# Kernel tuning notes

Measured on AMD Instinct MI355X. Metric: run time of the kernel, lower is better.

The kernel has to match this reference:

```python
import jax, jax.numpy as jnp
import numpy as np

B, S, D = 2, 2048, 2048
H = 16
HD = D // H  # 128
THETA = 10000.0


def setup_inputs() -> dict:
    key = jax.random.key(0)
    ks = jax.random.split(key, 5)
    return {
        "hidden_states": jax.random.normal(ks[0], (B, S, D), dtype=jnp.float32),
        "Wq": jax.random.normal(ks[1], (D, D), dtype=jnp.float32) * 0.02,
        "Wk": jax.random.normal(ks[2], (D, D), dtype=jnp.float32) * 0.02,
        "Wv": jax.random.normal(ks[3], (D, D), dtype=jnp.float32) * 0.02,
        "Wo": jax.random.normal(ks[4], (D, D), dtype=jnp.float32) * 0.02,
    }


def _rotate_half(x):
    x1, x2 = x[..., : HD // 2], x[..., HD // 2:]
    return jnp.concatenate([-x2, x1], axis=-1)


def _rope_cos_sin(seq_len, dtype):
    # freqs = 1/theta^(2i/d), i in [0, d/2)
    inv_freq = 1.0 / (THETA ** (jnp.arange(0, HD, 2, dtype=jnp.float32) / HD))
    ang = jnp.arange(seq_len, dtype=jnp.float32)[:, None] * inv_freq[None, :]  # [S, HD/2]
    cos = jnp.cos(ang).astype(dtype)
    sin = jnp.sin(ang).astype(dtype)
    # torch code does cos.repeat(1,1,1,2): tile halves -> [S, HD]
    cos2 = jnp.concatenate([cos, cos], axis=-1)[None, None]  # [1,1,S,HD]
    sin2 = jnp.concatenate([sin, sin], axis=-1)[None, None]
    return cos2, sin2


def reference(hidden_states, Wq, Wk, Wv, Wo):
    b, s, d = hidden_states.shape
    scale = 1.0 / np.sqrt(HD)
    # torch Linear: y = x @ W.T
    def proj(W):
        y = jnp.einsum("bsd,ed->bse", hidden_states, W)
        return y.reshape(b, s, H, HD).transpose(0, 2, 1, 3)  # [b,h,s,hd]
    q, k, v = proj(Wq), proj(Wk), proj(Wv)

    cos, sin = _rope_cos_sin(s, q.dtype)
    q = q * cos + _rotate_half(q) * sin
    k = k * cos + _rotate_half(k) * sin

    scores = jnp.einsum("bhqd,bhkd->bhqk", q, k) * scale
    # causal mask: -inf strictly above diagonal (kv_len == seq_len here)
    causal = jnp.triu(jnp.full((s, s), -jnp.inf, dtype=scores.dtype), k=1)
    scores = scores + causal[None, None]

    attn = jax.nn.softmax(scores.astype(jnp.float32), axis=-1).astype(q.dtype)
    ctx = jnp.einsum("bhqk,bhkd->bhqd", attn, v)
    ctx = ctx.transpose(0, 2, 1, 3).reshape(b, s, d)
    return jnp.einsum("bsd,ed->bse", ctx, Wo)
```

## Files before the change

### kernel.cpp

```cpp
#include <hip/hip_runtime.h>

typedef unsigned short ushort_t;
typedef __bf16 bf16x8 __attribute__((ext_vector_type(8)));
typedef float f32x4 __attribute__((ext_vector_type(4)));

#define S_LEN 2048
#define DMODEL 2048
#define NH 16
#define HDIM 128
#define BATCH 2
#define M_ROWS (BATCH * S_LEN)

__device__ __forceinline__ ushort_t f2bf(float f) {
    union { float f; unsigned u; } v; v.f = f;
    unsigned r = (v.u + 0x7fffu + ((v.u >> 16) & 1u)) >> 16;
    return (ushort_t)r;
}
__device__ __forceinline__ float bf2f(ushort_t u) {
    union { unsigned u; float f; } v; v.u = ((unsigned)u) << 16;
    return v.f;
}

__device__ __forceinline__ void async16(const void* g, void* l) {
    __builtin_amdgcn_global_load_lds(
        (const __attribute__((address_space(1))) void*)g,
        (__attribute__((address_space(3))) void*)l, 16, 0, 0);
}

__global__ void cvt_bf16(const float* __restrict__ in, ushort_t* __restrict__ out, int n4) {
    int i = blockIdx.x * blockDim.x + threadIdx.x;
    if (i >= n4) return;
    float4 f = ((const float4*)in)[i];
    ushort4 u;
    u.x = f2bf(f.x); u.y = f2bf(f.y); u.z = f2bf(f.z); u.w = f2bf(f.w);
    ((ushort4*)out)[i] = u;
}

__global__ void cvt4_bf16(const float* __restrict__ w0, const float* __restrict__ w1,
                          const float* __restrict__ w2, const float* __restrict__ w3,
                          ushort_t* __restrict__ out, int n4) {
    int i = blockIdx.x * blockDim.x + threadIdx.x;
    if (i >= n4) return;
    int which = blockIdx.y;
    const float* src = which == 0 ? w0 : which == 1 ? w1 : which == 2 ? w2 : w3;
    float4 f = ((const float4*)src)[i];
    ushort4 u;
    u.x = f2bf(f.x); u.y = f2bf(f.y); u.z = f2bf(f.z); u.w = f2bf(f.w);
    ((ushort4*)(out + (size_t)which * DMODEL * DMODEL))[i] = u;
}

__global__ void rope_tables(float* __restrict__ cosT, float* __restrict__ sinT) {
    int i = blockIdx.x * blockDim.x + threadIdx.x;
    int s = i >> 6, f = i & 63;
    float inv = powf(10000.0f, -(float)(2 * f) / 128.0f);
    float ang = (float)s * inv;
    cosT[i] = cosf(ang);
    sinT[i] = sinf(ang);
}

__global__ void rope_inplace(ushort_t* __restrict__ Q, ushort_t* __restrict__ K,
                             const float* __restrict__ cosT, const float* __restrict__ sinT) {
    long i = (long)blockIdx.x * blockDim.x + threadIdx.x;
    int f = (int)(i & 63);
    long t = i >> 6;
    int s = (int)(t & (S_LEN - 1));
    int bh = (int)(t >> 11);
    long base = ((long)bh * S_LEN + s) * HDIM;
    float c = cosT[s * 64 + f], sn = sinT[s * 64 + f];
    float a0 = bf2f(Q[base + f]), a1 = bf2f(Q[base + 64 + f]);
    Q[base + f]      = f2bf(a0 * c - a1 * sn);
    Q[base + 64 + f] = f2bf(a1 * c + a0 * sn);
    float b0 = bf2f(K[base + f]), b1 = bf2f(K[base + 64 + f]);
    K[base + f]      = f2bf(b0 * c - b1 * sn);
    K[base + 64 + f] = f2bf(b1 * c + b0 * sn);
}

__global__ __launch_bounds__(512) void gemm_qkv(
    const ushort_t* __restrict__ A, const ushort_t* __restrict__ Bm,
    ushort_t* __restrict__ Cq, ushort_t* __restrict__ Ck, ushort_t* __restrict__ Cv,
    int K) {
    __shared__ __align__(16) ushort_t As[2][256 * 64];
    __shared__ __align__(16) ushort_t Bs[2][192 * 64];
    const int tid = threadIdx.x;
    const int lane = tid & 63;
    const int w = tid >> 6;
    const int wm = w >> 2, wn = w & 3;
    const int fr = lane & 15, g = lane >> 4;
    const int xcd = blockIdx.x & 7;
    const int local = blockIdx.x >> 3;
    const int brow = (local >> 2) * 256;
    const int bcol = (xcd * 4 + (local & 3)) * 192;

    const ushort_t* aSrc[4];
    const ushort_t* bSrc[3];
    int aDst[4], bDst[3];
#pragma unroll
    for (int q = 0; q < 4; q++) {
        int d = (q * 512 + tid) * 16;
        int row = d >> 7;
        int s = d ^ ((row & 7) << 4);
        aSrc[q] = A + (long)(brow + row) * K + ((s & 127) >> 1);
        aDst[q] = (q * 512 + tid) * 8;
    }
#pragma unroll
    for (int q = 0; q < 3; q++) {
        int d = (q * 512 + tid) * 16;
        int row = d >> 7;
        int s = d ^ ((row & 7) << 4);
        bSrc[q] = Bm + (long)(bcol + row) * K + ((s & 127) >> 1);
        bDst[q] = (q * 512 + tid) * 8;
    }

    f32x4 acc[8][3];
#pragma unroll
    for (int m = 0; m < 8; m++)
#pragma unroll
        for (int n = 0; n < 3; n++) acc[m][n] = (f32x4){0.f, 0.f, 0.f, 0.f};

    auto stageEarly = [&](int buf, int k0) {
        async16(aSrc[0] + k0, &As[buf][aDst[0]]);
        async16(aSrc[2] + k0, &As[buf][aDst[2]]);
#pragma unroll
        for (int q = 0; q < 3; q++) async16(bSrc[q] + k0, &Bs[buf][bDst[q]]);
    };
    auto stageLate = [&](int buf, int k0) {
        async16(aSrc[1] + k0, &As[buf][aDst[1]]);
        async16(aSrc[3] + k0, &As[buf][aDst[3]]);
    };
    auto rdA = [&](int buf, int m, int ks) -> bf16x8 {
        int row = wm * 128 + m * 16 + fr;
        int cb = (ks * 64 + g * 16) ^ ((row & 7) << 4);
        return *(const bf16x8*)((const char*)&As[buf][0] + row * 128 + cb);
    };
    auto rdB = [&](int buf, int n, int ks) -> bf16x8 {
        int row = wn * 48 + n * 16 + fr;
        int cb = (ks * 64 + g * 16) ^ ((row & 7) << 4);
        return *(const bf16x8*)((const char*)&Bs[buf][0] + row * 128 + cb);
    };

    const int NT = K / 64;
    stageEarly(0, 0);  stageLate(0, 0);
    stageEarly(1, 64); stageLate(1, 64);

    for (int kt = 0; kt < NT; ++kt) {
        const int cur = kt & 1;
        if (kt + 1 < NT) asm volatile("s_waitcnt vmcnt(7)" ::: "memory");
        else             asm volatile("s_waitcnt vmcnt(0)" ::: "memory");
        __builtin_amdgcn_sched_barrier(0);
        __builtin_amdgcn_s_barrier();
        __builtin_amdgcn_sched_barrier(0);

        bf16x8 bfv[3][2], af[4][2];
#pragma unroll
        for (int n = 0; n < 3; n++)
#pragma unroll
            for (int ks = 0; ks < 2; ks++) bfv[n][ks] = rdB(cur, n, ks);
#pragma unroll
        for (int m = 0; m < 4; m++)
#pragma unroll
            for (int ks = 0; ks < 2; ks++) af[m][ks] = rdA(cur, m, ks);
        __builtin_amdgcn_s_setprio(1);
#pragma unroll
        for (int m = 0; m < 4; m++)
#pragma unroll
            for (int n = 0; n < 3; n++)
#pragma unroll
                for (int ks = 0; ks < 2; ks++)
                    acc[m][n] = __builtin_amdgcn_mfma_f32_16x16x32_bf16(af[m][ks], bfv[n][ks], acc[m][n], 0, 0, 0);
        __builtin_amdgcn_s_setprio(0);
        __builtin_amdgcn_s_barrier();
        __builtin_amdgcn_sched_barrier(0);
        if (kt + 2 < NT) stageEarly(cur, (kt + 2) * 64);

        bf16x8 af2[4][2];
#pragma unroll
        for (int m = 0; m < 4; m++)
#pragma unroll
            for (int ks = 0; ks < 2; ks++) af2[m][ks] = rdA(cur, m + 4, ks);
        __builtin_amdgcn_s_setprio(1);
#pragma unroll
        for (int m = 0; m < 4; m++)
#pragma unroll
            for (int n = 0; n < 3; n++)
#pragma unroll
                for (int ks = 0; ks < 2; ks++)
                    acc[m + 4][n] = __builtin_amdgcn_mfma_f32_16x16x32_bf16(af2[m][ks], bfv[n][ks], acc[m + 4][n], 0, 0, 0);
        __builtin_amdgcn_s_setprio(0);
        __builtin_amdgcn_s_barrier();
        __builtin_amdgcn_sched_barrier(0);
        if (kt + 2 < NT) stageLate(cur, (kt + 2) * 64);
    }

    const int rbase = brow + wm * 128;
#pragma unroll
    for (int n = 0; n < 3; n++) {
        int c2abs = bcol + wn * 48 + n * 16 + fr;
        int proj = c2abs >> 11;
        int c2 = c2abs & 2047;
        int h = c2 >> 7, hd = c2 & 127;
        if (proj < 2) {
            ushort_t* dst = proj == 0 ? Cq : Ck;
#pragma unroll
            for (int m = 0; m < 8; m++)
#pragma unroll
                for (int r = 0; r < 4; r++) {
                    int row = rbase + m * 16 + g * 4 + r;
                    int b = row >> 11, s = row & (S_LEN - 1);
                    dst[(((long)(b * NH + h) * S_LEN) + s) * HDIM + hd] = f2bf(acc[m][n][r]);
                }
        } else {
#pragma unroll
            for (int m = 0; m < 8; m++) {
                int row0 = rbase + m * 16 + g * 4;
                int b = row0 >> 11, s0 = row0 & (S_LEN - 1);
                ushort4 u;
                u.x = f2bf(acc[m][n][0]); u.y = f2bf(acc[m][n][1]);
                u.z = f2bf(acc[m][n][2]); u.w = f2bf(acc[m][n][3]);
                *(ushort4*)&Cv[(((long)(b * NH + h) * HDIM) + hd) * S_LEN + s0] = u;
            }
        }
    }
}

__global__ __launch_bounds__(256) void gemm128_o(
    const ushort_t* __restrict__ A, const ushort_t* __restrict__ Bm,
    float* __restrict__ C0, int NB, int K) {
    __shared__ __align__(16) ushort_t As[2][128 * 64];
    __shared__ __align__(16) ushort_t Bs[2][128 * 64];
    const int tid = threadIdx.x;
    const int lane = tid & 63;
    const int w = tid >> 6;
    const int fr = lane & 15, g = lane >> 4;
    const int cpx = NB >> 3;
    const int xcd = blockIdx.x & 7;
    const int local = blockIdx.x >> 3;
    const int brow = (local / cpx) * 128;
    const int bcol = (xcd * cpx + local % cpx) * 128;

    const ushort_t* aSrc[4]; const ushort_t* bSrc[4];
    int aDst[4], bDst[4];
#pragma unroll
    for (int q = 0; q < 4; q++) {
        int d = (q * 256 + tid) * 16;
        int row = d >> 7;
        int s = d ^ ((row & 7) << 4);
        aSrc[q] = A + (long)(brow + row) * K + ((s & 127) >> 1);
        bSrc[q] = Bm + (long)(bcol + row) * K + ((s & 127) >> 1);
        aDst[q] = bDst[q] = (q * 256 + tid) * 8;
    }

    f32x4 acc[8][2];
#pragma unroll
    for (int m = 0; m < 8; m++)
#pragma unroll
        for (int n = 0; n < 2; n++) acc[m][n] = (f32x4){0.f, 0.f, 0.f, 0.f};

    auto stage = [&](int buf, int k0) {
#pragma unroll
        for (int q = 0; q < 4; q++) async16(aSrc[q] + k0, &As[buf][aDst[q]]);
#pragma unroll
        for (int q = 0; q < 4; q++) async16(bSrc[q] + k0, &Bs[buf][bDst[q]]);
    };
    auto rdA = [&](int buf, int m, int ks) -> bf16x8 {
        int row = m * 16 + fr;
        int cb = (ks * 64 + g * 16) ^ ((row & 7) << 4);
        return *(const bf16x8*)((const char*)&As[buf][0] + row * 128 + cb);
    };
    auto rdB = [&](int buf, int n, int ks) -> bf16x8 {
        int row = w * 32 + n * 16 + fr;
        int cb = (ks * 64 + g * 16) ^ ((row & 7) << 4);
        return *(const bf16x8*)((const char*)&Bs[buf][0] + row * 128 + cb);
    };

    const int NT = K / 64;
    stage(0, 0);
    stage(1, 64);

    for (int kt = 0; kt < NT; ++kt) {
        const int cur = kt & 1;
        if (kt + 1 < NT) asm volatile("s_waitcnt vmcnt(8)" ::: "memory");
        else             asm volatile("s_waitcnt vmcnt(0)" ::: "memory");
        __builtin_amdgcn_sched_barrier(0);
        __builtin_amdgcn_s_barrier();
        __builtin_amdgcn_sched_barrier(0);

        bf16x8 bfv[2][2], af[8][2];
#pragma unroll
        for (int n = 0; n < 2; n++)
#pragma unroll
            for (int ks = 0; ks < 2; ks++) bfv[n][ks] = rdB(cur, n, ks);
#pragma unroll
        for (int m = 0; m < 8; m++)
#pragma unroll
            for (int ks = 0; ks < 2; ks++) af[m][ks] = rdA(cur, m, ks);
        __builtin_amdgcn_s_setprio(1);
#pragma unroll
        for (int m = 0; m < 8; m++)
#pragma unroll
            for (int n = 0; n < 2; n++)
#pragma unroll
                for (int ks = 0; ks < 2; ks++)
                    acc[m][n] = __builtin_amdgcn_mfma_f32_16x16x32_bf16(af[m][ks], bfv[n][ks], acc[m][n], 0, 0, 0);
        __builtin_amdgcn_s_setprio(0);

        __builtin_amdgcn_s_barrier();
        __builtin_amdgcn_sched_barrier(0);
        if (kt + 2 < NT) stage(cur, (kt + 2) * 64);
    }

#pragma unroll
    for (int m = 0; m < 8; m++)
#pragma unroll
        for (int n = 0; n < 2; n++) {
            int col = bcol + w * 32 + n * 16 + fr;
#pragma unroll
            for (int r = 0; r < 4; r++) {
                int row = brow + m * 16 + g * 4 + r;
                C0[(long)row * DMODEL + col] = acc[m][n][r];
            }
        }
}

__global__ __launch_bounds__(256) void attn_fwd_v4(
    const ushort_t* __restrict__ Q, const ushort_t* __restrict__ K,
    const ushort_t* __restrict__ Vt, ushort_t* __restrict__ ctx) {
    __shared__ __align__(16) ushort_t Ks[2][64 * 128];
    __shared__ __align__(16) ushort_t Vs[2][128 * 64];
    __shared__ __align__(16) ushort_t Pls[4][16 * 64];

    const int tid = threadIdx.x;
    const int lane = tid & 63;
    const int w = tid >> 6;
    const int g = lane >> 4;
    const int fr = lane & 15;
    const int fk = g * 8;

    const int bid = blockIdx.x;
    const int xcd = bid & 7;
    const int t6 = bid >> 3;
    const int bh = xcd + 8 * (t6 & 3);
    const int p = t6 >> 2;
    const int qtA = p, qtB = 31 - p;
    const int b = bh >> 4, h = bh & 15;

    const ushort_t* Qb = Q + (long)bh * S_LEN * HDIM;
    const ushort_t* Kb = K + (long)bh * S_LEN * HDIM;
    const ushort_t* Vb = Vt + (long)bh * HDIM * S_LEN;

    int koff[4], voff[4], kdst[4], vdst[4];
#pragma unroll
    for (int r = 0; r < 4; r++) {
        int ci = r * 256 + tid;
        int krow = ci >> 4, kwc = ci & 15;
        koff[r] = krow * HDIM + ((kwc ^ (krow & 7)) * 8);
        kdst[r] = ci * 8;
        int vrow = ci >> 3, vwc = ci & 7;
        voff[r] = vrow * S_LEN + ((vwc ^ (vrow & 7)) * 8);
        vdst[r] = ci * 8;
    }
    auto stage = [&](int buf, int kv0) {
        const ushort_t* Kg = Kb + (long)kv0 * HDIM;
        const ushort_t* Vg = Vb + kv0;
#pragma unroll
        for (int r = 0; r < 4; r++) async16(Kg + koff[r], &Ks[buf][kdst[r]]);
#pragma unroll
        for (int r = 0; r < 4; r++) async16(Vg + voff[r], &Vs[buf][vdst[r]]);
    };

    int qrow0 = qtA * 64 + w * 16;
    bf16x8 qf[4];
    auto loadQ = [&]() {
#pragma unroll
        for (int t = 0; t < 4; t++)
            qf[t] = *(const bf16x8*)&Qb[(long)(qrow0 + fr) * HDIM + t * 32 + fk];
    };
    loadQ();

    f32x4 o[8];
#pragma unroll
    for (int i = 0; i < 8; i++) o[i] = (f32x4){0.f, 0.f, 0.f, 0.f};
    float mrun = -1e30f, lrun = 0.f;

    const float scale = 0.08838834764831845f;
    long obase = ((long)b * S_LEN) * DMODEL + (long)h * HDIM;
    auto flush = [&]() {
        float inv = 1.0f / lrun;
        long rowb = obase + (long)(qrow0 + fr) * DMODEL;
#pragma unroll
        for (int dt = 0; dt < 8; dt++) {
            ushort4 u;
            u.x = f2bf(o[dt][0] * inv); u.y = f2bf(o[dt][1] * inv);
            u.z = f2bf(o[dt][2] * inv); u.w = f2bf(o[dt][3] * inv);
            *(ushort4*)&ctx[rowb + dt * 16 + g * 4] = u;
        }
    };

    const int ntA = qtA + 1;
    const int ntot = 33;

    stage(0, 0);
    __syncthreads();

    int cur = 0;
    for (int u = 0; u < ntot; ++u) {
        if (u + 1 < ntot) {
            int kvn = (u + 1 < ntA) ? (u + 1) : (u + 1 - ntA);
            stage(cur ^ 1, kvn * 64);
        }
        const int kv0 = ((u < ntA) ? u : (u - ntA)) * 64;
        if (u == ntA) {
            flush();
            qrow0 = qtB * 64 + w * 16;
            loadQ();
#pragma unroll
            for (int i = 0; i < 8; i++) o[i] = (f32x4){0.f, 0.f, 0.f, 0.f};
            mrun = -1e30f; lrun = 0.f;
        }
        if (kv0 <= qrow0 + 15) {
            f32x4 sf[4];
#pragma unroll
            for (int c = 0; c < 4; c++) sf[c] = (f32x4){0.f, 0.f, 0.f, 0.f};
            __builtin_amdgcn_s_setprio(1);
#pragma unroll
            for (int c = 0; c < 4; c++) {
                const int krow = c * 16 + fr;
#pragma unroll
                for (int tt = 0; tt < 4; tt++) {
                    bf16x8 kb = *(const bf16x8*)&Ks[cur][krow * 128 + (((tt * 4 + g) ^ (krow & 7)) * 8)];
                    sf[c] = __builtin_amdgcn_mfma_f32_16x16x32_bf16(kb, qf[tt], sf[c], 0, 0, 0);
                }
            }
            __builtin_amdgcn_s_setprio(0);
            if (kv0 + 63 <= qrow0) {
#pragma unroll
                for (int c = 0; c < 4; c++)
#pragma unroll
                    for (int r = 0; r < 4; r++) sf[c][r] *= scale;
            } else {
                const int q = qrow0 + fr;
#pragma unroll
                for (int c = 0; c < 4; c++)
#pragma unroll
                    for (int r = 0; r < 4; r++) {
                        int kv = kv0 + c * 16 + g * 4 + r;
                        sf[c][r] = (kv <= q) ? sf[c][r] * scale : -1e30f;
                    }
            }
            {
                float vmax = -1e30f;
#pragma unroll
                for (int c = 0; c < 4; c++) {
                    float t0 = fmaxf(fmaxf(sf[c][0], sf[c][1]), fmaxf(sf[c][2], sf[c][3]));
                    vmax = fmaxf(vmax, t0);
                }
                vmax = fmaxf(vmax, __shfl_xor(vmax, 16));
                vmax = fmaxf(vmax, __shfl_xor(vmax, 32));
                if (!__all(vmax - mrun <= 8.f)) {
                    float nm = fmaxf(mrun, vmax);
                    float alpha = __expf(mrun - nm);
                    mrun = nm;
                    lrun *= alpha;
#pragma unroll
                    for (int dt = 0; dt < 8; dt++) o[dt] *= alpha;
                }
                float rs = 0.f;
#pragma unroll
                for (int c = 0; c < 4; c++)
#pragma unroll
                    for (int r = 0; r < 4; r++) {
                        float pv = __expf(sf[c][r] - mrun);
                        sf[c][r] = pv;
                        rs += pv;
                    }
                rs += __shfl_xor(rs, 16);
                rs += __shfl_xor(rs, 32);
                lrun += rs;
            }
#pragma unroll
            for (int c = 0; c < 4; c++) {
                ushort4 u;
                u.x = f2bf(sf[c][0]); u.y = f2bf(sf[c][1]);
                u.z = f2bf(sf[c][2]); u.w = f2bf(sf[c][3]);
                *(ushort4*)&Pls[w][fr * 64 + ((c * 16 + g * 4) ^ ((fr & 7) << 3))] = u;
            }
            bf16x8 pa[2];
#pragma unroll
            for (int hh = 0; hh < 2; hh++)
                pa[hh] = *(const bf16x8*)&Pls[w][fr * 64 + ((hh * 32 + g * 8) ^ ((fr & 7) << 3))];
            __builtin_amdgcn_s_setprio(1);
#pragma unroll
            for (int dt = 0; dt < 8; dt++) {
                const int vrow = dt * 16 + fr;
#pragma unroll
                for (int hh = 0; hh < 2; hh++) {
                    bf16x8 vb = *(const bf16x8*)&Vs[cur][vrow * 64 + (((hh * 4 + g) ^ (vrow & 7)) * 8)];
                    o[dt] = __builtin_amdgcn_mfma_f32_16x16x32_bf16(vb, pa[hh], o[dt], 0, 0, 0);
                }
            }
            __builtin_amdgcn_s_setprio(0);
        }
        __syncthreads();
        cur ^= 1;
    }
    flush();
}

extern "C" void kernel_launch(void* const* d_in, const int* in_sizes, int n_in,
                              void* d_out, int out_size, void* d_ws, size_t ws_size,
                              hipStream_t stream) {
    const float* hs = (const float*)d_in[0];
    const float* Wq = (const float*)d_in[1];
    const float* Wk = (const float*)d_in[2];
    const float* Wv = (const float*)d_in[3];
    const float* Wo = (const float*)d_in[4];
    float* out = (float*)d_out;

    size_t off = 0;
    char* wsb = (char*)d_ws;
    auto carve = [&](size_t bytes) { void* p = wsb + off; off += bytes; return p; };

    ushort_t* Xb   = (ushort_t*)carve((size_t)M_ROWS * DMODEL * 2);
    ushort_t* Wqb  = (ushort_t*)carve((size_t)DMODEL * DMODEL * 2);
    ushort_t* Wkb  = (ushort_t*)carve((size_t)DMODEL * DMODEL * 2);
    ushort_t* Wvb  = (ushort_t*)carve((size_t)DMODEL * DMODEL * 2);
    ushort_t* Wob  = (ushort_t*)carve((size_t)DMODEL * DMODEL * 2);
    ushort_t* Qb   = (ushort_t*)carve((size_t)BATCH * NH * S_LEN * HDIM * 2);
    ushort_t* Kb   = (ushort_t*)carve((size_t)BATCH * NH * S_LEN * HDIM * 2);
    ushort_t* Vtb  = (ushort_t*)carve((size_t)BATCH * NH * S_LEN * HDIM * 2);
    ushort_t* ctxb = (ushort_t*)carve((size_t)M_ROWS * DMODEL * 2);
    float* cosT    = (float*)carve((size_t)S_LEN * 64 * 4);
    float* sinT    = (float*)carve((size_t)S_LEN * 64 * 4);

    const int nX = M_ROWS * DMODEL;
    const int nW = DMODEL * DMODEL;

    cvt_bf16<<<(nX / 4) / 256, 256, 0, stream>>>(hs, Xb, nX / 4);
    cvt4_bf16<<<dim3((nW / 4) / 256, 4), 256, 0, stream>>>(Wq, Wk, Wv, Wo, Wqb, nW / 4);
    rope_tables<<<(S_LEN * 64) / 256, 256, 0, stream>>>(cosT, sinT);

    gemm_qkv<<<512, 512, 0, stream>>>(Xb, Wqb, Qb, Kb, Vtb, DMODEL);

    rope_inplace<<<(BATCH * NH * S_LEN * 64) / 256, 256, 0, stream>>>(Qb, Kb, cosT, sinT);

    attn_fwd_v4<<<512, 256, 0, stream>>>(Qb, Kb, Vtb, ctxb);

    gemm128_o<<<(M_ROWS / 128) * (DMODEL / 128), 256, 0, stream>>>(
        ctxb, Wob, out, DMODEL / 128, DMODEL);
}
```

Before: 282.1 us.

## Retile QKV GEMM to 128x256 blocks with 4 waves and BK=32

Replaces the 512-thread 256x192 QKV GEMM tile (BK=64, XOR-swizzled LDS, split early/late staging) with a 256-thread 128x256 tile using BK=32. Each wave now owns a 128x64 output sub-tile, and one stage loads everything per k-step. The LDS swizzle is dropped. The grid grows from 512 to 768 blocks so the 96 column tiles are spread evenly across the XCDs. The aim is better occupancy and load balance, at the cost of possible LDS bank conflicts from the unswizzled 64-byte rows and twice as many barriers per unit of K.

```diff
diff --git a/kernel.cpp b/kernel.cpp
--- a/kernel.cpp
+++ b/kernel.cpp
@@ -75,143 +75,113 @@
     K[base + 64 + f] = f2bf(b1 * c + b0 * sn);
 }
 
-__global__ __launch_bounds__(512) void gemm_qkv(
+__global__ __launch_bounds__(256) void gemm_qkv4(
     const ushort_t* __restrict__ A, const ushort_t* __restrict__ Bm,
     ushort_t* __restrict__ Cq, ushort_t* __restrict__ Ck, ushort_t* __restrict__ Cv,
     int K) {
-    __shared__ __align__(16) ushort_t As[2][256 * 64];
-    __shared__ __align__(16) ushort_t Bs[2][192 * 64];
+    __shared__ __align__(16) ushort_t As[2][128 * 32];
+    __shared__ __align__(16) ushort_t Bs[2][256 * 32];
     const int tid = threadIdx.x;
     const int lane = tid & 63;
     const int w = tid >> 6;
-    const int wm = w >> 2, wn = w & 3;
     const int fr = lane & 15, g = lane >> 4;
     const int xcd = blockIdx.x & 7;
     const int local = blockIdx.x >> 3;
-    const int brow = (local >> 2) * 256;
-    const int bcol = (xcd * 4 + (local & 3)) * 192;
-
-    const ushort_t* aSrc[4];
-    const ushort_t* bSrc[3];
-    int aDst[4], bDst[3];
+    const int brow = (local / 3) * 128;
+    const int bcol = (xcd * 3 + local % 3) * 256;
+
+    const ushort_t* aSrc[2];
+    const ushort_t* bSrc[4];
+    int aDst[2], bDst[4];
+#pragma unroll
+    for (int q = 0; q < 2; q++) {
+        int d = (q * 256 + tid) * 16;
+        int row = d >> 6;
+        aSrc[q] = A + (long)(brow + row) * K + ((d & 63) >> 1);
+        aDst[q] = (q * 256 + tid) * 8;
+    }
 #pragma unroll
     for (int q = 0; q < 4; q++) {
-        int d = (q * 512 + tid) * 16;
-        int row = d >> 7;
-        int s = d ^ ((row & 7) << 4);
-        aSrc[q] = A + (long)(brow + row) * K + ((s & 127) >> 1);
-        aDst[q] = (q * 512 + tid) * 8;
-    }
-#pragma unroll
-    for (int q = 0; q < 3; q++) {
-        int d = (q * 512 + tid) * 16;
-        int row = d >> 7;
-        int s = d ^ ((row & 7) << 4);
-        bSrc[q] = Bm + (long)(bcol + row) * K + ((s & 127) >> 1);
-        bDst[q] = (q * 512 + tid) * 8;
-    }
-
-    f32x4 acc[8][3];
+        int d = (q * 256 + tid) * 16;
+        int row = d >> 6;
+        bSrc[q] = Bm + (long)(bcol + row) * K + ((d & 63) >> 1);
+        bDst[q] = (q * 256 + tid) * 8;
+    }
+
+    f32x4 acc[8][4];
 #pragma unroll
     for (int m = 0; m < 8; m++)
 #pragma unroll
-        for (int n = 0; n < 3; n++) acc[m][n] = (f32x4){0.f, 0.f, 0.f, 0.f};
-
-    auto stageEarly = [&](int buf, int k0) {
-        async16(aSrc[0] + k0, &As[buf][aDst[0]]);
-        async16(aSrc[2] + k0, &As[buf][aDst[2]]);
-#pragma unroll
-        for (int q = 0; q < 3; q++) async16(bSrc[q] + k0, &Bs[buf][bDst[q]]);
-    };
-    auto stageLate = [&](int buf, int k0) {
-        async16(aSrc[1] + k0, &As[buf][aDst[1]]);
-        async16(aSrc[3] + k0, &As[buf][aDst[3]]);
-    };
-    auto rdA = [&](int buf, int m, int ks) -> bf16x8 {
-        int row = wm * 128 + m * 16 + fr;
-        int cb = (ks * 64 + g * 16) ^ ((row & 7) << 4);
-        return *(const bf16x8*)((const char*)&As[buf][0] + row * 128 + cb);
-    };
-    auto rdB = [&](int buf, int n, int ks) -> bf16x8 {
-        int row = wn * 48 + n * 16 + fr;
-        int cb = (ks * 64 + g * 16) ^ ((row & 7) << 4);
-        return *(const bf16x8*)((const char*)&Bs[buf][0] + row * 128 + cb);
-    };
-
-    const int NT = K / 64;
-    stageEarly(0, 0);  stageLate(0, 0);
-    stageEarly(1, 64); stageLate(1, 64);
+        for (int n = 0; n < 4; n++) acc[m][n] = (f32x4){0.f, 0.f, 0.f, 0.f};
+
+    auto stage = [&](int buf, int k0) {
+#pragma unroll
+        for (int q = 0; q < 2; q++) async16(aSrc[q] + k0, &As[buf][aDst[q]]);
+#pragma unroll
+        for (int q = 0; q < 4; q++) async16(bSrc[q] + k0, &Bs[buf][bDst[q]]);
+    };
+    auto rdA = [&](int buf, int m) -> bf16x8 {
+        return *(const bf16x8*)&As[buf][(m * 16 + fr) * 32 + g * 8];
+    };
+    auto rdB = [&](int buf, int n) -> bf16x8 {
+        return *(const bf16x8*)&Bs[buf][(w * 64 + n * 16 + fr) * 32 + g * 8];
+    };
+
+    const int NT = K / 32;
+    stage(0, 0);
+    stage(1, 32);
 
     for (int kt = 0; kt < NT; ++kt) {
         const int cur = kt & 1;
-        if (kt + 1 < NT) asm volatile("s_waitcnt vmcnt(7)" ::: "memory");
+        if (kt + 1 < NT) asm volatile("s_waitcnt vmcnt(6)" ::: "memory");
         else             asm volatile("s_waitcnt vmcnt(0)" ::: "memory");
         __builtin_amdgcn_sched_barrier(0);
         __builtin_amdgcn_s_barrier();
         __builtin_amdgcn_sched_barrier(0);
 
-        bf16x8 bfv[3][2], af[4][2];
-#pragma unroll
-        for (int n = 0; n < 3; n++)
-#pragma unroll
-            for (int ks = 0; ks < 2; ks++) bfv[n][ks] = rdB(cur, n, ks);
-#pragma unroll
-        for (int m = 0; m < 4; m++)
-#pragma unroll
-            for (int ks = 0; ks < 2; ks++) af[m][ks] = rdA(cur, m, ks);
+        bf16x8 bfv[4], af[8];
+#pragma unroll
+        for (int n = 0; n < 4; n++) bfv[n] = rdB(cur, n);
+#pragma unroll
+        for (int m = 0; m < 8; m++) af[m] = rdA(cur, m);
         __builtin_amdgcn_s_setprio(1);
 #pragma unroll
-        for (int m = 0; m < 4; m++)
-#pragma unroll
-            for (int n = 0; n < 3; n++)
-#pragma unroll
-                for (int ks = 0; ks < 2; ks++)
-                    acc[m][n] = __builtin_amdgcn_mfma_f32_16x16x32_bf16(af[m][ks], bfv[n][ks], acc[m][n], 0, 0, 0);
+        for (int m = 0; m < 8; m++)
+#pragma unroll
+            for (int n = 0; n < 4; n++)
+                acc[m][n] = __builtin_amdgcn_mfma_f32_16x16x32_bf16(af[m], bfv[n], acc[m][n], 0, 0, 0);
         __builtin_amdgcn_s_setprio(0);
+
         __builtin_amdgcn_s_barrier();
         __builtin_amdgcn_sched_barrier(0);
-        if (kt + 2 < NT) stageEarly(cur, (kt + 2) * 64);
-
-        bf16x8 af2[4][2];
-#pragma unroll
-        for (int m = 0; m < 4; m++)
-#pragma unroll
-            for (int ks = 0; ks < 2; ks++) af2[m][ks] = rdA(cur, m + 4, ks);
-        __builtin_amdgcn_s_setprio(1);
-#pragma unroll
-        for (int m = 0; m < 4; m++)
-#pragma unroll
-            for (int n = 0; n < 3; n++)
-#pragma unroll
-                for (int ks = 0; ks < 2; ks++)
-                    acc[m + 4][n] = __builtin_amdgcn_mfma_f32_16x16x32_bf16(af2[m][ks], bfv[n][ks], acc[m + 4][n], 0, 0, 0);
-        __builtin_amdgcn_s_setprio(0);
-        __builtin_amdgcn_s_barrier();
-        __builtin_amdgcn_sched_barrier(0);
-        if (kt + 2 < NT) stageLate(cur, (kt + 2) * 64);
-    }
-
-    const int rbase = brow + wm * 128;
-#pragma unroll
-    for (int n = 0; n < 3; n++) {
-        int c2abs = bcol + wn * 48 + n * 16 + fr;
-        int proj = c2abs >> 11;
-        int c2 = c2abs & 2047;
-        int h = c2 >> 7, hd = c2 & 127;
-        if (proj < 2) {
-            ushort_t* dst = proj == 0 ? Cq : Ck;
+        if (kt + 2 < NT) stage(cur, (kt + 2) * 32);
+    }
+
+    const int proj = bcol >> 11;
+    const int cbase = (bcol & 2047) + w * 64;
+    if (proj < 2) {
+        ushort_t* dst = proj == 0 ? Cq : Ck;
+#pragma unroll
+        for (int n = 0; n < 4; n++) {
+            int c2 = cbase + n * 16 + fr;
+            int h = c2 >> 7, hd = c2 & 127;
 #pragma unroll
             for (int m = 0; m < 8; m++)
 #pragma unroll
                 for (int r = 0; r < 4; r++) {
-                    int row = rbase + m * 16 + g * 4 + r;
+                    int row = brow + m * 16 + g * 4 + r;
                     int b = row >> 11, s = row & (S_LEN - 1);
                     dst[(((long)(b * NH + h) * S_LEN) + s) * HDIM + hd] = f2bf(acc[m][n][r]);
                 }
-        } else {
+        }
+    } else {
+#pragma unroll
+        for (int n = 0; n < 4; n++) {
+            int c2 = cbase + n * 16 + fr;
+            int h = c2 >> 7, hd = c2 & 127;
 #pragma unroll
             for (int m = 0; m < 8; m++) {
-                int row0 = rbase + m * 16 + g * 4;
+                int row0 = brow + m * 16 + g * 4;
                 int b = row0 >> 11, s0 = row0 & (S_LEN - 1);
                 ushort4 u;
                 u.x = f2bf(acc[m][n][0]); u.y = f2bf(acc[m][n][1]);
@@ -538,7 +508,7 @@
     cvt4_bf16<<<dim3((nW / 4) / 256, 4), 256, 0, stream>>>(Wq, Wk, Wv, Wo, Wqb, nW / 4);
     rope_tables<<<(S_LEN * 64) / 256, 256, 0, stream>>>(cosT, sinT);
 
-    gemm_qkv<<<512, 512, 0, stream>>>(Xb, Wqb, Qb, Kb, Vtb, DMODEL);
+    gemm_qkv4<<<768, 256, 0, stream>>>(Xb, Wqb, Qb, Kb, Vtb, DMODEL);
 
     rope_inplace<<<(BATCH * NH * S_LEN * 64) / 256, 256, 0, stream>>>(Qb, Kb, cosT, sinT);
 
```

Result: slower. 341.6 us (+21.1%).

## Restage QKV GEMM into eight interleaved phases, retile O GEMM, use exp2 softmax

Applied to the files above, without the earlier changes.

The QKV projection GEMM loop is split into four MFMA quarters, one per k-substep and half-tile, separated by barriers. Its A and B tile prefetches are interleaved between these quarters, and a 2-blocks-per-CU launch bound is requested. The output GEMM switches from 1x4 to 2x2 wave tiling, so each wave reuses a 64x64 block of A and B fragments. The attention softmax folds log2(e) into the scale, uses exp2f, and widens the rescale threshold to match. The changes aim to improve overlap and fragment reuse, but add more barriers. The occupancy hint may also raise register pressure, since the LDS footprint likely still limits the kernel to one block per CU.

```diff
diff --git a/kernel.cpp b/kernel.cpp
--- a/kernel.cpp
+++ b/kernel.cpp
@@ -75,7 +75,7 @@
     K[base + 64 + f] = f2bf(b1 * c + b0 * sn);
 }
 
-__global__ __launch_bounds__(512) void gemm_qkv(
+__global__ __launch_bounds__(512, 2) void gemm_qkv8(
     const ushort_t* __restrict__ A, const ushort_t* __restrict__ Bm,
     ushort_t* __restrict__ Cq, ushort_t* __restrict__ Ck, ushort_t* __restrict__ Cv,
     int K) {
@@ -91,8 +91,7 @@
     const int brow = (local >> 2) * 256;
     const int bcol = (xcd * 4 + (local & 3)) * 192;
 
-    const ushort_t* aSrc[4];
-    const ushort_t* bSrc[3];
+    const ushort_t* aSrc[4]; const ushort_t* bSrc[3];
     int aDst[4], bDst[3];
 #pragma unroll
     for (int q = 0; q < 4; q++) {
@@ -117,15 +116,13 @@
 #pragma unroll
         for (int n = 0; n < 3; n++) acc[m][n] = (f32x4){0.f, 0.f, 0.f, 0.f};
 
-    auto stageEarly = [&](int buf, int k0) {
-        async16(aSrc[0] + k0, &As[buf][aDst[0]]);
-        async16(aSrc[2] + k0, &As[buf][aDst[2]]);
+    auto stageA = [&](int buf, int k0) {
+#pragma unroll
+        for (int q = 0; q < 4; q++) async16(aSrc[q] + k0, &As[buf][aDst[q]]);
+    };
+    auto stageB = [&](int buf, int k0) {
 #pragma unroll
         for (int q = 0; q < 3; q++) async16(bSrc[q] + k0, &Bs[buf][bDst[q]]);
-    };
-    auto stageLate = [&](int buf, int k0) {
-        async16(aSrc[1] + k0, &As[buf][aDst[1]]);
-        async16(aSrc[3] + k0, &As[buf][aDst[3]]);
     };
     auto rdA = [&](int buf, int m, int ks) -> bf16x8 {
         int row = wm * 128 + m * 16 + fr;
@@ -139,56 +136,83 @@
     };
 
     const int NT = K / 64;
-    stageEarly(0, 0);  stageLate(0, 0);
-    stageEarly(1, 64); stageLate(1, 64);
+    stageA(0, 0);  stageB(0, 0);
+    stageA(1, 64); stageB(1, 64);
 
     for (int kt = 0; kt < NT; ++kt) {
         const int cur = kt & 1;
+        __builtin_amdgcn_sched_barrier(0);
         if (kt + 1 < NT) asm volatile("s_waitcnt vmcnt(7)" ::: "memory");
         else             asm volatile("s_waitcnt vmcnt(0)" ::: "memory");
         __builtin_amdgcn_sched_barrier(0);
         __builtin_amdgcn_s_barrier();
         __builtin_amdgcn_sched_barrier(0);
 
-        bf16x8 bfv[3][2], af[4][2];
-#pragma unroll
-        for (int n = 0; n < 3; n++)
-#pragma unroll
-            for (int ks = 0; ks < 2; ks++) bfv[n][ks] = rdB(cur, n, ks);
-#pragma unroll
-        for (int m = 0; m < 4; m++)
-#pragma unroll
-            for (int ks = 0; ks < 2; ks++) af[m][ks] = rdA(cur, m, ks);
+        bf16x8 af0[4][2], af1[4][2], bfv[3][2];
+#pragma unroll
+        for (int m = 0; m < 4; m++)
+#pragma unroll
+            for (int ks = 0; ks < 2; ks++) af0[m][ks] = rdA(cur, m, ks);
+#pragma unroll
+        for (int n = 0; n < 3; n++) bfv[n][0] = rdB(cur, n, 0);
+        __builtin_amdgcn_sched_barrier(0);
+        __builtin_amdgcn_s_barrier();
+        __builtin_amdgcn_sched_barrier(0);
         __builtin_amdgcn_s_setprio(1);
 #pragma unroll
         for (int m = 0; m < 4; m++)
 #pragma unroll
             for (int n = 0; n < 3; n++)
-#pragma unroll
-                for (int ks = 0; ks < 2; ks++)
-                    acc[m][n] = __builtin_amdgcn_mfma_f32_16x16x32_bf16(af[m][ks], bfv[n][ks], acc[m][n], 0, 0, 0);
+                acc[m][n] = __builtin_amdgcn_mfma_f32_16x16x32_bf16(af0[m][0], bfv[n][0], acc[m][n], 0, 0, 0);
         __builtin_amdgcn_s_setprio(0);
-        __builtin_amdgcn_s_barrier();
-        __builtin_amdgcn_sched_barrier(0);
-        if (kt + 2 < NT) stageEarly(cur, (kt + 2) * 64);
-
-        bf16x8 af2[4][2];
-#pragma unroll
-        for (int m = 0; m < 4; m++)
-#pragma unroll
-            for (int ks = 0; ks < 2; ks++) af2[m][ks] = rdA(cur, m + 4, ks);
+        __builtin_amdgcn_sched_barrier(0);
+        __builtin_amdgcn_s_barrier();
+        __builtin_amdgcn_sched_barrier(0);
+#pragma unroll
+        for (int m = 0; m < 4; m++)
+#pragma unroll
+            for (int ks = 0; ks < 2; ks++) af1[m][ks] = rdA(cur, m + 4, ks);
+#pragma unroll
+        for (int n = 0; n < 3; n++) bfv[n][1] = rdB(cur, n, 1);
+        __builtin_amdgcn_sched_barrier(0);
+        __builtin_amdgcn_s_barrier();
+        __builtin_amdgcn_sched_barrier(0);
         __builtin_amdgcn_s_setprio(1);
 #pragma unroll
         for (int m = 0; m < 4; m++)
 #pragma unroll
             for (int n = 0; n < 3; n++)
-#pragma unroll
-                for (int ks = 0; ks < 2; ks++)
-                    acc[m + 4][n] = __builtin_amdgcn_mfma_f32_16x16x32_bf16(af2[m][ks], bfv[n][ks], acc[m + 4][n], 0, 0, 0);
+                acc[m + 4][n] = __builtin_amdgcn_mfma_f32_16x16x32_bf16(af1[m][0], bfv[n][0], acc[m + 4][n], 0, 0, 0);
         __builtin_amdgcn_s_setprio(0);
-        __builtin_amdgcn_s_barrier();
-        __builtin_amdgcn_sched_barrier(0);
-        if (kt + 2 < NT) stageLate(cur, (kt + 2) * 64);
+        __builtin_amdgcn_sched_barrier(0);
+        __builtin_amdgcn_s_barrier();
+        __builtin_amdgcn_sched_barrier(0);
+        if (kt + 2 < NT) stageA(cur, (kt + 2) * 64);
+        __builtin_amdgcn_sched_barrier(0);
+        __builtin_amdgcn_s_barrier();
+        __builtin_amdgcn_sched_barrier(0);
+        __builtin_amdgcn_s_setprio(1);
+#pragma unroll
+        for (int m = 0; m < 4; m++)
+#pragma unroll
+            for (int n = 0; n < 3; n++)
+                acc[m][n] = __builtin_amdgcn_mfma_f32_16x16x32_bf16(af0[m][1], bfv[n][1], acc[m][n], 0, 0, 0);
+        __builtin_amdgcn_s_setprio(0);
+        __builtin_amdgcn_sched_barrier(0);
+        __builtin_amdgcn_s_barrier();
+        __builtin_amdgcn_sched_barrier(0);
+        if (kt + 2 < NT) stageB(cur, (kt + 2) * 64);
+        __builtin_amdgcn_sched_barrier(0);
+        __builtin_amdgcn_s_barrier();
+        __builtin_amdgcn_sched_barrier(0);
+        __builtin_amdgcn_s_setprio(1);
+#pragma unroll
+        for (int m = 0; m < 4; m++)
+#pragma unroll
+            for (int n = 0; n < 3; n++)
+                acc[m + 4][n] = __builtin_amdgcn_mfma_f32_16x16x32_bf16(af1[m][1], bfv[n][1], acc[m + 4][n], 0, 0, 0);
+        __builtin_amdgcn_s_setprio(0);
+        __builtin_amdgcn_sched_barrier(0);
     }
 
     const int rbase = brow + wm * 128;
@@ -230,6 +254,7 @@
     const int tid = threadIdx.x;
     const int lane = tid & 63;
     const int w = tid >> 6;
+    const int wm = w >> 1, wn = w & 1;
     const int fr = lane & 15, g = lane >> 4;
     const int cpx = NB >> 3;
     const int xcd = blockIdx.x & 7;
@@ -249,11 +274,11 @@
         aDst[q] = bDst[q] = (q * 256 + tid) * 8;
     }
 
-    f32x4 acc[8][2];
-#pragma unroll
-    for (int m = 0; m < 8; m++)
-#pragma unroll
-        for (int n = 0; n < 2; n++) acc[m][n] = (f32x4){0.f, 0.f, 0.f, 0.f};
+    f32x4 acc[4][4];
+#pragma unroll
+    for (int m = 0; m < 4; m++)
+#pragma unroll
+        for (int n = 0; n < 4; n++) acc[m][n] = (f32x4){0.f, 0.f, 0.f, 0.f};
 
     auto stage = [&](int buf, int k0) {
 #pragma unroll
@@ -262,12 +287,12 @@
         for (int q = 0; q < 4; q++) async16(bSrc[q] + k0, &Bs[buf][bDst[q]]);
     };
     auto rdA = [&](int buf, int m, int ks) -> bf16x8 {
-        int row = m * 16 + fr;
+        int row = wm * 64 + m * 16 + fr;
         int cb = (ks * 64 + g * 16) ^ ((row & 7) << 4);
         return *(const bf16x8*)((const char*)&As[buf][0] + row * 128 + cb);
     };
     auto rdB = [&](int buf, int n, int ks) -> bf16x8 {
-        int row = w * 32 + n * 16 + fr;
+        int row = wn * 64 + n * 16 + fr;
         int cb = (ks * 64 + g * 16) ^ ((row & 7) << 4);
         return *(const bf16x8*)((const char*)&Bs[buf][0] + row * 128 + cb);
     };
@@ -284,20 +309,20 @@
         __builtin_amdgcn_s_barrier();
         __builtin_amdgcn_sched_barrier(0);
 
-        bf16x8 bfv[2][2], af[8][2];
-#pragma unroll
-        for (int n = 0; n < 2; n++)
+        bf16x8 bfv[4][2], af[4][2];
+#pragma unroll
+        for (int n = 0; n < 4; n++)
 #pragma unroll
             for (int ks = 0; ks < 2; ks++) bfv[n][ks] = rdB(cur, n, ks);
 #pragma unroll
-        for (int m = 0; m < 8; m++)
+        for (int m = 0; m < 4; m++)
 #pragma unroll
             for (int ks = 0; ks < 2; ks++) af[m][ks] = rdA(cur, m, ks);
         __builtin_amdgcn_s_setprio(1);
 #pragma unroll
-        for (int m = 0; m < 8; m++)
-#pragma unroll
-            for (int n = 0; n < 2; n++)
+        for (int m = 0; m < 4; m++)
+#pragma unroll
+            for (int n = 0; n < 4; n++)
 #pragma unroll
                 for (int ks = 0; ks < 2; ks++)
                     acc[m][n] = __builtin_amdgcn_mfma_f32_16x16x32_bf16(af[m][ks], bfv[n][ks], acc[m][n], 0, 0, 0);
@@ -309,13 +334,13 @@
     }
 
 #pragma unroll
-    for (int m = 0; m < 8; m++)
-#pragma unroll
-        for (int n = 0; n < 2; n++) {
-            int col = bcol + w * 32 + n * 16 + fr;
+    for (int m = 0; m < 4; m++)
+#pragma unroll
+        for (int n = 0; n < 4; n++) {
+            int col = bcol + wn * 64 + n * 16 + fr;
 #pragma unroll
             for (int r = 0; r < 4; r++) {
-                int row = brow + m * 16 + g * 4 + r;
+                int row = brow + wm * 64 + m * 16 + g * 4 + r;
                 C0[(long)row * DMODEL + col] = acc[m][n][r];
             }
         }
@@ -381,7 +406,7 @@
     for (int i = 0; i < 8; i++) o[i] = (f32x4){0.f, 0.f, 0.f, 0.f};
     float mrun = -1e30f, lrun = 0.f;
 
-    const float scale = 0.08838834764831845f;
+    const float scale2 = 0.08838834764831845f * 1.4426950408889634f;
     long obase = ((long)b * S_LEN) * DMODEL + (long)h * HDIM;
     auto flush = [&]() {
         float inv = 1.0f / lrun;
@@ -435,7 +460,7 @@
 #pragma unroll
                 for (int c = 0; c < 4; c++)
 #pragma unroll
-                    for (int r = 0; r < 4; r++) sf[c][r] *= scale;
+                    for (int r = 0; r < 4; r++) sf[c][r] *= scale2;
             } else {
                 const int q = qrow0 + fr;
 #pragma unroll
@@ -443,7 +468,7 @@
 #pragma unroll
                     for (int r = 0; r < 4; r++) {
                         int kv = kv0 + c * 16 + g * 4 + r;
-                        sf[c][r] = (kv <= q) ? sf[c][r] * scale : -1e30f;
+                        sf[c][r] = (kv <= q) ? sf[c][r] * scale2 : -1e30f;
                     }
             }
             {
@@ -455,9 +480,9 @@
                 }
                 vmax = fmaxf(vmax, __shfl_xor(vmax, 16));
                 vmax = fmaxf(vmax, __shfl_xor(vmax, 32));
-                if (!__all(vmax - mrun <= 8.f)) {
+                if (!__all(vmax - mrun <= 11.5f)) {
                     float nm = fmaxf(mrun, vmax);
-                    float alpha = __expf(mrun - nm);
+                    float alpha = exp2f(mrun - nm);
                     mrun = nm;
                     lrun *= alpha;
 #pragma unroll
@@ -468,7 +493,7 @@
                 for (int c = 0; c < 4; c++)
 #pragma unroll
                     for (int r = 0; r < 4; r++) {
-                        float pv = __expf(sf[c][r] - mrun);
+                        float pv = exp2f(sf[c][r] - mrun);
                         sf[c][r] = pv;
                         rs += pv;
                     }
@@ -478,10 +503,10 @@
             }
 #pragma unroll
             for (int c = 0; c < 4; c++) {
-                ushort4 u;
-                u.x = f2bf(sf[c][0]); u.y = f2bf(sf[c][1]);
-                u.z = f2bf(sf[c][2]); u.w = f2bf(sf[c][3]);
-                *(ushort4*)&Pls[w][fr * 64 + ((c * 16 + g * 4) ^ ((fr & 7) << 3))] = u;
+                ushort4 u2;
+                u2.x = f2bf(sf[c][0]); u2.y = f2bf(sf[c][1]);
+                u2.z = f2bf(sf[c][2]); u2.w = f2bf(sf[c][3]);
+                *(ushort4*)&Pls[w][fr * 64 + ((c * 16 + g * 4) ^ ((fr & 7) << 3))] = u2;
             }
             bf16x8 pa[2];
 #pragma unroll
@@ -538,7 +563,7 @@
     cvt4_bf16<<<dim3((nW / 4) / 256, 4), 256, 0, stream>>>(Wq, Wk, Wv, Wo, Wqb, nW / 4);
     rope_tables<<<(S_LEN * 64) / 256, 256, 0, stream>>>(cosT, sinT);
 
-    gemm_qkv<<<512, 512, 0, stream>>>(Xb, Wqb, Qb, Kb, Vtb, DMODEL);
+    gemm_qkv8<<<512, 512, 0, stream>>>(Xb, Wqb, Qb, Kb, Vtb, DMODEL);
 
     rope_inplace<<<(BATCH * NH * S_LEN * 64) / 256, 256, 0, stream>>>(Qb, Kb, cosT, sinT);
 
```

Measured after the change: 269.5 us. -4.5%, faster.
